# Performance work log

Hardware: AMD Instinct MI355X
Metric: run time of the kernel (lower is better)

Reference implementation:

```python
import jax, jax.numpy as jnp
import numpy as np
from jax import lax

NVOX = 100
EPS = 1e-4
DN = ('NDHWC', 'DHWIO', 'NDHWC')

# scn semantics emulated densely: inactive voxels are identically zero and the
# active-site mask is re-applied after every layer, so submanifold convolution,
# strided sparse conv, sparse deconv and masked BN-ReLU compute the same values
# at active sites as SparseConvNet's rulebook gather-GEMM-scatter.

def _bnrelu(x, p, mask):
    # p: [4, C] = (gamma, beta, running_mean, running_var); inference-form BN.
    g, b, mu, v = p[0], p[1], p[2], p[3]
    return jax.nn.relu((x - mu) * (g * lax.rsqrt(v + EPS)) + b) * mask

def _subconv(x, w, mask):
    # Submanifold conv: inputs outside active set are zero; outputs only at active sites.
    return lax.conv_general_dilated(x, w, (1, 1, 1), 'SAME', dimension_numbers=DN) * mask

def _down(x, w):
    # scn.Convolution(dim, a, b, size=2, stride=2, bias=False)
    return lax.conv_general_dilated(x, w, (2, 2, 2), 'VALID', dimension_numbers=DN)

def _up(x, w, mask):
    # scn.Deconvolution restores the pre-downsample active set -> mask with finer mask.
    return lax.conv_transpose(x, w, (2, 2, 2), 'VALID', dimension_numbers=DN) * mask

def _pool_mask(mask):
    return lax.reduce_window(mask, 0.0, lax.max, (1, 2, 2, 2, 1), (1, 2, 2, 2, 1), 'VALID')

def _forward(coords, feats, w_in, w0a, wdown0, w1a, wdown1, w2, wup1, w1post, wup0, w0post,
             bnA, bnB, bnC, bnD, bnE, bnF, bnG, bnH, bnI, bnJ, linW, linb):
    i, j, k = coords[:, 0], coords[:, 1], coords[:, 2]
    # InputLayer mode=3: sum features at duplicate coordinates.
    grid = jnp.zeros((1, NVOX, NVOX, NVOX, 1), feats.dtype).at[0, i, j, k, 0].add(feats[:, 0])
    mask0 = jnp.zeros((1, NVOX, NVOX, NVOX, 1), feats.dtype).at[0, i, j, k, 0].set(1.0)
    mask1 = _pool_mask(mask0)   # 50^3 active set after strided conv
    mask2 = _pool_mask(mask1)   # 25^3

    x = _subconv(grid, w_in, mask0)                          # 1 -> 32
    x0 = _subconv(_bnrelu(x, bnA, mask0), w0a, mask0)        # level-0 VGG block
    d0 = _down(_bnrelu(x0, bnB, mask0), wdown0)              # 32 -> 64, 100 -> 50
    x1 = _subconv(_bnrelu(d0, bnC, mask1), w1a, mask1)       # level-1 VGG block
    d1 = _down(_bnrelu(x1, bnD, mask1), wdown1)              # 64 -> 96, 50 -> 25
    x2 = _subconv(_bnrelu(d1, bnE, mask2), w2, mask2)        # level-2 VGG block
    u1 = _up(_bnrelu(x2, bnF, mask2), wup1, mask1)           # 96 -> 64, 25 -> 50
    y1 = _subconv(_bnrelu(jnp.concatenate([x1, u1], -1), bnG, mask1), w1post, mask1)  # 128 -> 64
    u0 = _up(_bnrelu(y1, bnH, mask1), wup0, mask0)           # 64 -> 32, 50 -> 100
    y0 = _subconv(_bnrelu(jnp.concatenate([x0, u0], -1), bnI, mask0), w0post, mask0)  # 64 -> 32
    y = _bnrelu(y0, bnJ, mask0)                              # final BatchNormReLU(32)
    pts = y[0, i, j, k, :]                                   # OutputLayer: gather active sites [N,32]
    return pts @ linW + linb                                 # Linear(32, 3)


def setup_inputs() -> dict:
    key = jax.random.key(0)
    ks = jax.random.split(key, 24)
    N = 120000
    coords = jax.random.randint(ks[0], (N, 3), 0, NVOX, dtype=jnp.int32)
    feats = jax.random.normal(ks[1], (N, 1), jnp.float32)

    def w(k, shape, fan_in):
        return (jax.random.normal(k, shape, jnp.float32) / np.float32(np.sqrt(fan_in)))

    def bn(k, c):
        k1, k2, k3, k4 = jax.random.split(k, 4)
        return jnp.stack([
            1.0 + 0.1 * jax.random.normal(k1, (c,)),
            0.1 * jax.random.normal(k2, (c,)),
            0.1 * jax.random.normal(k3, (c,)),
            0.5 + jax.random.uniform(k4, (c,)),
        ]).astype(jnp.float32)

    return dict(
        coords=coords, feats=feats,
        w_in=w(ks[2], (3, 3, 3, 1, 32), 27),
        w0a=w(ks[3], (3, 3, 3, 32, 32), 27 * 32),
        wdown0=w(ks[4], (2, 2, 2, 32, 64), 8 * 32),
        w1a=w(ks[5], (3, 3, 3, 64, 64), 27 * 64),
        wdown1=w(ks[6], (2, 2, 2, 64, 96), 8 * 64),
        w2=w(ks[7], (3, 3, 3, 96, 96), 27 * 96),
        wup1=w(ks[8], (2, 2, 2, 96, 64), 96),
        w1post=w(ks[9], (3, 3, 3, 128, 64), 27 * 128),
        wup0=w(ks[10], (2, 2, 2, 64, 32), 64),
        w0post=w(ks[11], (3, 3, 3, 64, 32), 27 * 64),
        bnA=bn(ks[12], 32), bnB=bn(ks[13], 32), bnC=bn(ks[14], 64), bnD=bn(ks[15], 64),
        bnE=bn(ks[16], 96), bnF=bn(ks[17], 96), bnG=bn(ks[18], 128), bnH=bn(ks[19], 64),
        bnI=bn(ks[20], 64), bnJ=bn(ks[21], 32),
        linW=w(ks[22], (32, 3), 32),
        linb=0.01 * jax.random.normal(ks[23], (3,), jnp.float32),
    )


def reference(coords, feats, w_in, w0a, wdown0, w1a, wdown1, w2, wup1, w1post, wup0, w0post,
              bnA, bnB, bnC, bnD, bnE, bnF, bnG, bnH, bnI, bnJ, linW, linb):
    return _forward(coords, feats, w_in, w0a, wdown0, w1a, wdown1, w2, wup1, w1post, wup0, w0post,
                    bnA, bnB, bnC, bnD, bnE, bnF, bnG, bnH, bnI, bnJ, linW, linb)
```

## Files before the change

kernel.cpp:

```cpp
#include <hip/hip_runtime.h>


#define NVOX 100
#define EPSB 1e-4f
typedef unsigned long long u64;
typedef _Float16 h2 __attribute__((ext_vector_type(2)));
typedef _Float16 h8 __attribute__((ext_vector_type(8)));
typedef float f16v __attribute__((ext_vector_type(16)));
#define DEVFN __device__ __forceinline__

DEVFN float bnr(float v, float sc, float sh) { return fmaxf(fmaf(v, sc, sh), 0.f); }

template<int NTAPS, int CTOT, int COUT>
__global__ __launch_bounds__(256)
void prepB32(const float* __restrict__ w, h2* __restrict__ out)
{
    constexpr int CTG = COUT / 32, KCH = CTOT / 16;
    const int n = NTAPS * CTG * KCH * 256;
    const int idx = blockIdx.x * 256 + threadIdx.x;
    if (idx >= n) return;
    const int jh = idx & 3;
    const int lane = (idx >> 2) & 63;
    int r = idx >> 8;
    const int kc = r % KCH; r /= KCH;
    const int ct = r % CTG; const int t = r / CTG;
    const int k0 = kc * 16 + (lane >> 5) * 8 + 2 * jh;
    const int co = ct * 32 + (lane & 31);
    h2 v;
    v[0] = (_Float16)w[((size_t)t * CTOT + k0) * COUT + co];
    v[1] = (_Float16)w[((size_t)t * CTOT + k0 + 1) * COUT + co];
    out[idx] = v;
}

template<int EMODE, int COUT>
DEVFN void epilogue(float a, int srow, int ch,
                    float* outF, _Float16* o1, const float* sc1, const float* sh1,
                    _Float16* o2, const float* sc2, const float* sh2)
{
    if constexpr (EMODE == 0) {
        outF[(size_t)srow * COUT + ch] = a;
    } else {
        o1[(size_t)srow * COUT + ch] = (_Float16)bnr(a, sc1[ch], sh1[ch]);
        if constexpr (EMODE == 2)
            o2[(size_t)srow * COUT + ch] = (_Float16)bnr(a, sc2[ch], sh2[ch]);
    }
}

template<int KC1, int KC2, int CTILES, int COUT, int S, int EMODE>
__global__ __launch_bounds__(64)
void gconv_m32(const h2* __restrict__ inA, const h2* __restrict__ inB,
               const h2* __restrict__ wb,
               const int* __restrict__ amap, const int* __restrict__ vlist,
               const int* __restrict__ cnt, int cap, int nbx,
               float* __restrict__ outF, _Float16* __restrict__ o1,
               const float* __restrict__ sc1, const float* __restrict__ sh1,
               _Float16* __restrict__ o2,
               const float* __restrict__ sc2, const float* __restrict__ sh2)
{
    constexpr int KCH = KC1 + KC2;
    constexpr int CTG = COUT / 32;
    const int lane = threadIdx.x;
    const int cntv = *cnt;
    const int sid = blockIdx.x;
    const int ct0 = sid / nbx;
    const int wbase = (sid - ct0 * nbx) * 32;
    if (wbase >= cntv) return;
    const int l31 = lane & 31, ksub = lane >> 5;
    const int slot = wbase + l31;
    const bool on = slot < cntv;
    int X = 0, Y = 0, Z = 0;
    if (on) { const int v = vlist[slot]; X = v % S; const int r = v / S; Y = r % S; Z = r / S; }

    auto calc_ns = [&](int t) -> int {
        int ns = cap;
        if (on) {
            const int dz = t / 9 - 1, dy = (t / 3) % 3 - 1, dx = t % 3 - 1;
            const int nz = Z + dz, ny = Y + dy, nx = X + dx;
            if ((unsigned)nz < (unsigned)S && (unsigned)ny < (unsigned)S &&
                (unsigned)nx < (unsigned)S) {
                const int m = amap[(nz * S + ny) * S + nx];
                if (m >= 0) ns = m;
            }
        }
        return ns;
    };

    f16v acc[CTILES];
#pragma unroll
    for (int c = 0; c < CTILES; ++c) acc[c] = (f16v)(0.f);
    int ns = calc_ns(0);
#pragma unroll 1
    for (int t = 0; t < 27; ++t) {
        const int ns_nxt = (t + 1 < 27) ? calc_ns(t + 1) : cap;
        const h2* __restrict__ wt =
            wb + ((size_t)t * CTG + ct0 * CTILES) * KCH * 256;
#pragma unroll
        for (int kc = 0; kc < KC1; ++kc) {
            const h8 a = *reinterpret_cast<const h8*>(
                inA + (size_t)ns * (KC1 * 8) + kc * 8 + ksub * 4);
#pragma unroll
            for (int ct = 0; ct < CTILES; ++ct) {
                const h8 b = *reinterpret_cast<const h8*>(
                    wt + ((size_t)ct * KCH + kc) * 256 + lane * 4);
                acc[ct] = __builtin_amdgcn_mfma_f32_32x32x16_f16(a, b, acc[ct], 0, 0, 0);
            }
        }
        if constexpr (KC2 > 0) {
#pragma unroll
            for (int kc = 0; kc < KC2; ++kc) {
                const h8 a = *reinterpret_cast<const h8*>(
                    inB + (size_t)ns * (KC2 * 8) + kc * 8 + ksub * 4);
#pragma unroll
                for (int ct = 0; ct < CTILES; ++ct) {
                    const h8 b = *reinterpret_cast<const h8*>(
                        wt + ((size_t)ct * KCH + KC1 + kc) * 256 + lane * 4);
                    acc[ct] = __builtin_amdgcn_mfma_f32_32x32x16_f16(a, b, acc[ct], 0, 0, 0);
                }
            }
        }
        ns = ns_nxt;
    }
#pragma unroll
    for (int ct = 0; ct < CTILES; ++ct) {
        const int ch = (ct0 * CTILES + ct) * 32 + l31;
#pragma unroll
        for (int r = 0; r < 16; ++r) {
            const int row = (r & 3) + 8 * (r >> 2) + 4 * ksub;
            const int srow = wbase + row;
            if (srow < cntv)
                epilogue<EMODE, COUT>(acc[ct][r], srow, ch, outF, o1, sc1, sh1,
                                      o2, sc2, sh2);
        }
    }
}

template<int KCH, int CTILES, int COUT, int SC>
__global__ __launch_bounds__(64)
void dconv_m32(const h2* __restrict__ in, const h2* __restrict__ wb,
               const int* __restrict__ amap_f, const int* __restrict__ vlist_c,
               const int* __restrict__ cnt_c, int capf, int nbx,
               _Float16* __restrict__ o1,
               const float* __restrict__ sc1, const float* __restrict__ sh1)
{
    constexpr int SF = SC * 2;
    constexpr int CTG = COUT / 32;
    const int lane = threadIdx.x;
    const int cntv = *cnt_c;
    const int sid = blockIdx.x;
    const int ct0 = sid / nbx;
    const int wbase = (sid - ct0 * nbx) * 32;
    if (wbase >= cntv) return;
    const int l31 = lane & 31, ksub = lane >> 5;
    const int slot = wbase + l31;
    const bool on = slot < cntv;
    int X = 0, Y = 0, Z = 0;
    if (on) { const int v = vlist_c[slot]; X = v % SC; const int r = v / SC; Y = r % SC; Z = r / SC; }

    auto calc_ns = [&](int t) -> int {
        int ns = capf;
        if (on) {
            const int fz = 2 * Z + ((t >> 2) & 1);
            const int fy = 2 * Y + ((t >> 1) & 1);
            const int fx = 2 * X + (t & 1);
            const int m = amap_f[(fz * SF + fy) * SF + fx];
            if (m >= 0) ns = m;
        }
        return ns;
    };

    f16v acc[CTILES];
#pragma unroll
    for (int c = 0; c < CTILES; ++c) acc[c] = (f16v)(0.f);
    int ns = calc_ns(0);
#pragma unroll 1
    for (int t = 0; t < 8; ++t) {
        const int ns_nxt = (t + 1 < 8) ? calc_ns(t + 1) : capf;
        const h2* __restrict__ wt =
            wb + ((size_t)t * CTG + ct0 * CTILES) * KCH * 256;
#pragma unroll
        for (int kc = 0; kc < KCH; ++kc) {
            const h8 a = *reinterpret_cast<const h8*>(
                in + (size_t)ns * (KCH * 8) + kc * 8 + ksub * 4);
#pragma unroll
            for (int ct = 0; ct < CTILES; ++ct) {
                const h8 b = *reinterpret_cast<const h8*>(
                    wt + ((size_t)ct * KCH + kc) * 256 + lane * 4);
                acc[ct] = __builtin_amdgcn_mfma_f32_32x32x16_f16(a, b, acc[ct], 0, 0, 0);
            }
        }
        ns = ns_nxt;
    }
#pragma unroll
    for (int ct = 0; ct < CTILES; ++ct) {
        const int ch = (ct0 * CTILES + ct) * 32 + l31;
#pragma unroll
        for (int r = 0; r < 16; ++r) {
            const int row = (r & 3) + 8 * (r >> 2) + 4 * ksub;
            const int srow = wbase + row;
            if (srow < cntv)
                o1[(size_t)srow * COUT + ch] =
                    (_Float16)bnr(acc[ct][r], sc1[ch], sh1[ch]);
        }
    }
}

template<int KCH, int CTILES, int COUT, int SC>
__global__ __launch_bounds__(64)
void uconv_m32(const h2* __restrict__ in, const h2* __restrict__ wb,
               const int* __restrict__ amap_f, const int* __restrict__ vlist_c,
               const int* __restrict__ cnt_c, int cap, int nbx,
               _Float16* __restrict__ out,
               const float* __restrict__ sc, const float* __restrict__ sh)
{
    constexpr int SF = SC * 2;
    constexpr int CTG = COUT / 32;
    const int lane = threadIdx.x;
    const int cntv = *cnt_c;
    const int sid = blockIdx.x;
    const int ct0 = sid / nbx;
    const int wbase = (sid - ct0 * nbx) * 32;
    if (wbase >= cntv) return;
    const int l31 = lane & 31, ksub = lane >> 5;
    const int slot = wbase + l31;
    const bool on = slot < cntv;
    int X = 0, Y = 0, Z = 0;
    if (on) { const int v = vlist_c[slot]; X = v % SC; const int r = v / SC; Y = r % SC; Z = r / SC; }

    h8 a[KCH];
    const int arow = on ? slot : cap;
#pragma unroll
    for (int kc = 0; kc < KCH; ++kc)
        a[kc] = *reinterpret_cast<const h8*>(
            in + (size_t)arow * (KCH * 8) + kc * 8 + ksub * 4);

    auto calc_cs = [&](int t) -> int {
        int cs = -1;
        if (on) {
            const int fz = 2 * Z + ((t >> 2) & 1);
            const int fy = 2 * Y + ((t >> 1) & 1);
            const int fx = 2 * X + (t & 1);
            cs = amap_f[(fz * SF + fy) * SF + fx];
        }
        return cs;
    };

    int cs = calc_cs(0);
#pragma unroll 1
    for (int t = 0; t < 8; ++t) {
        const int cs_nxt = (t + 1 < 8) ? calc_cs(t + 1) : -1;
        const h2* __restrict__ wt =
            wb + ((size_t)(7 - t) * CTG + ct0 * CTILES) * KCH * 256;
        f16v acc[CTILES];
#pragma unroll
        for (int c = 0; c < CTILES; ++c) acc[c] = (f16v)(0.f);
#pragma unroll
        for (int kc = 0; kc < KCH; ++kc) {
#pragma unroll
            for (int ct = 0; ct < CTILES; ++ct) {
                const h8 b = *reinterpret_cast<const h8*>(
                    wt + ((size_t)ct * KCH + kc) * 256 + lane * 4);
                acc[ct] = __builtin_amdgcn_mfma_f32_32x32x16_f16(a[kc], b, acc[ct], 0, 0, 0);
            }
        }
#pragma unroll
        for (int ct = 0; ct < CTILES; ++ct) {
            const int ch = (ct0 * CTILES + ct) * 32 + l31;
#pragma unroll
            for (int r = 0; r < 16; ++r) {
                const int row = (r & 3) + 8 * (r >> 2) + 4 * ksub;
                const int csr = __shfl(cs, row, 64);
                if (csr >= 0)
                    out[(size_t)csr * COUT + ch] =
                        (_Float16)bnr(acc[ct][r], sc[ch], sh[ch]);
            }
        }
        cs = cs_nxt;
    }
}

template<int S>
__global__ __launch_bounds__(128)
void cin_k(const float* __restrict__ grid, const float* __restrict__ w,
           const int* __restrict__ vlist, const int* __restrict__ cnt,
           _Float16* __restrict__ out, const float* __restrict__ sc,
           const float* __restrict__ sh)
{
    const int wOff = __builtin_amdgcn_readfirstlane(threadIdx.x >> 6) * 16;
    const int slot = blockIdx.x * 64 + (threadIdx.x & 63);
    if (slot >= *cnt) return;
    const int v = vlist[slot];
    const int x = v % S;
    const int rem = v / S;
    const int y = rem % S;
    const int z = rem / S;
    float acc[16];
#pragma unroll
    for (int c = 0; c < 16; ++c) acc[c] = 0.f;
#pragma unroll
    for (int t = 0; t < 27; ++t) {
        const int dz = t / 9 - 1, dy = (t / 3) % 3 - 1, dx = t % 3 - 1;
        const int nz = z + dz, ny = y + dy, nx = x + dx;
        if ((unsigned)nz >= (unsigned)S || (unsigned)ny >= (unsigned)S ||
            (unsigned)nx >= (unsigned)S) continue;
        const float val = grid[(nz * S + ny) * S + nx];
        const float* __restrict__ wp = w + t * 32 + wOff;
#pragma unroll
        for (int c = 0; c < 16; ++c) acc[c] = fmaf(val, wp[c], acc[c]);
    }
    union { float4 v[2]; _Float16 h[16]; } o;
#pragma unroll
    for (int c = 0; c < 16; ++c)
        o.h[c] = (_Float16)bnr(acc[c], sc[wOff + c], sh[wOff + c]);
    float4* dst = reinterpret_cast<float4*>(out + (size_t)slot * 32 + wOff);
    dst[0] = o.v[0];
    dst[1] = o.v[1];
}

__global__ __launch_bounds__(256)
void final_k(const int* __restrict__ coords, const float* __restrict__ y0,
             const int* __restrict__ amap0, const float* __restrict__ ssJ,
             const float* __restrict__ linW, const float* __restrict__ linb,
             int N, float* __restrict__ outp)
{
    const int n = blockIdx.x * blockDim.x + threadIdx.x;
    if (n >= N) return;
    const int i = coords[3 * n + 0];
    const int j = coords[3 * n + 1];
    const int k = coords[3 * n + 2];
    const int v = (i * NVOX + j) * NVOX + k;
    const int s = amap0[v];
    float a0 = linb[0], a1 = linb[1], a2 = linb[2];
    if (s >= 0) {
        const float* __restrict__ row = y0 + (size_t)s * 32;
#pragma unroll
        for (int c = 0; c < 32; ++c) {
            const float t = bnr(row[c], ssJ[c], ssJ[32 + c]);
            a0 = fmaf(t, linW[c * 3 + 0], a0);
            a1 = fmaf(t, linW[c * 3 + 1], a1);
            a2 = fmaf(t, linW[c * 3 + 2], a2);
        }
    }
    outp[3 * n + 0] = a0;
    outp[3 * n + 1] = a1;
    outp[3 * n + 2] = a2;
}

__global__ void bn_prep(const float* __restrict__ A, const float* __restrict__ B,
                        const float* __restrict__ C, const float* __restrict__ D,
                        const float* __restrict__ E, const float* __restrict__ F,
                        const float* __restrict__ G, const float* __restrict__ H,
                        const float* __restrict__ I, const float* __restrict__ J,
                        float* __restrict__ ss)
{
    const float* bp[10] = {A, B, C, D, E, F, G, H, I, J};
    const int CH[10] = {32, 32, 64, 64, 96, 96, 128, 64, 64, 32};
    int idx = blockIdx.x * blockDim.x + threadIdx.x;
    if (idx >= 672) return;
    int l = 0, base = 0, off2 = 0;
    while (idx >= base + CH[l]) { base += CH[l]; off2 += 2 * CH[l]; ++l; }
    const int c = idx - base;
    const float* bn = bp[l];
    const int Cc = CH[l];
    const float g = bn[c], b = bn[Cc + c], mu = bn[2 * Cc + c], var = bn[3 * Cc + c];
    const float sc = g * rsqrtf(var + EPSB);
    ss[off2 + c] = sc;
    ss[off2 + Cc + c] = b - mu * sc;
}

__global__ __launch_bounds__(256)
void scatter_mark(const int* __restrict__ coords, const float* __restrict__ feats,
                  int N, float* __restrict__ grid, int* __restrict__ amap0)
{
    const int n = blockIdx.x * blockDim.x + threadIdx.x;
    if (n >= N) return;
    const int i = coords[3 * n + 0];
    const int j = coords[3 * n + 1];
    const int k = coords[3 * n + 2];
    const int v = (i * NVOX + j) * NVOX + k;
    atomicAdd(&grid[v], feats[n]);
    amap0[v] = -2;
}

template<int SC>
__global__ __launch_bounds__(256)
void flag_coarse(const int* __restrict__ amap_f, int* __restrict__ amap_c)
{
    constexpr int SF = SC * 2;
    const int v = blockIdx.x * blockDim.x + threadIdx.x;
    if (v >= SC * SC * SC) return;
    const int x = v % SC;
    const int rem = v / SC;
    const int y = rem % SC;
    const int z = rem / SC;
    bool any = false;
#pragma unroll
    for (int t = 0; t < 8; ++t) {
        const int fz = 2 * z + ((t >> 2) & 1);
        const int fy = 2 * y + ((t >> 1) & 1);
        const int fx = 2 * x + (t & 1);
        if (amap_f[(fz * SF + fy) * SF + fx] >= 0) any = true;
    }
    amap_c[v] = any ? -2 : -1;
}

__global__ __launch_bounds__(256)
void count_k(const int* __restrict__ flags, int V, int* __restrict__ counts)
{
    const int v = blockIdx.x * 256 + threadIdx.x;
    const bool act = (v < V) && (flags[v] == -2);
    const u64 m = __ballot(act);
    __shared__ int c[4];
    const int wid = threadIdx.x >> 6;
    if ((threadIdx.x & 63) == 0) c[wid] = __popcll(m);
    __syncthreads();
    if (threadIdx.x == 0) counts[blockIdx.x] = c[0] + c[1] + c[2] + c[3];
}

__global__ __launch_bounds__(1024)
void scan_k(int* __restrict__ counts, int nb, int* __restrict__ total)
{
    __shared__ int sums[1024];
    const int t = threadIdx.x;
    int v[4];
    int s = 0;
#pragma unroll
    for (int i = 0; i < 4; ++i) {
        const int idx = t * 4 + i;
        v[i] = (idx < nb) ? counts[idx] : 0;
        s += v[i];
    }
    sums[t] = s;
    __syncthreads();
    for (int d = 1; d < 1024; d <<= 1) {
        const int add = (t >= d) ? sums[t - d] : 0;
        __syncthreads();
        sums[t] += add;
        __syncthreads();
    }
    int base = (t > 0) ? sums[t - 1] : 0;
#pragma unroll
    for (int i = 0; i < 4; ++i) {
        const int idx = t * 4 + i;
        if (idx < nb) counts[idx] = base;
        base += v[i];
    }
    if (t == 1023) *total = sums[1023];
}

__global__ __launch_bounds__(256)
void emit_k(int* __restrict__ amap, int V, const int* __restrict__ offsets,
            int* __restrict__ vlist)
{
    const int v = blockIdx.x * 256 + threadIdx.x;
    const bool act = (v < V) && (amap[v] == -2);
    const u64 m = __ballot(act);
    __shared__ int wbase[4];
    const int wid = threadIdx.x >> 6;
    const int lane = threadIdx.x & 63;
    if (lane == 0) wbase[wid] = __popcll(m);
    __syncthreads();
    if (threadIdx.x == 0) {
        int s = 0;
#pragma unroll
        for (int i = 0; i < 4; ++i) { const int t = wbase[i]; wbase[i] = s; s += t; }
    }
    __syncthreads();
    if (act) {
        const int slot = offsets[blockIdx.x] + wbase[wid] +
                         __popcll(m & ((1ull << lane) - 1ull));
        amap[v] = slot;
        vlist[slot] = v;
    }
}

extern "C" void kernel_launch(void* const* d_in, const int* in_sizes, int n_in,
                              void* d_out, int out_size, void* d_ws, size_t ws_size,
                              hipStream_t stream) {
    const int*   coords = (const int*)d_in[0];
    const float* feats  = (const float*)d_in[1];
    const float* w_in   = (const float*)d_in[2];
    const float* w0a    = (const float*)d_in[3];
    const float* wdown0 = (const float*)d_in[4];
    const float* w1a    = (const float*)d_in[5];
    const float* wdown1 = (const float*)d_in[6];
    const float* w2     = (const float*)d_in[7];
    const float* wup1   = (const float*)d_in[8];
    const float* w1post = (const float*)d_in[9];
    const float* wup0   = (const float*)d_in[10];
    const float* w0post = (const float*)d_in[11];
    const float* linW = (const float*)d_in[22];
    const float* linb = (const float*)d_in[23];
    float* outp = (float*)d_out;

    const int N = in_sizes[1];
    const int V0 = NVOX * NVOX * NVOX;
    const int V1 = 50 * 50 * 50;
    const int V2 = 25 * 25 * 25;
    const int cap0 = N;
    const int cap1 = 100000;
    const int cap2 = V2;

    char* ws = (char*)d_ws;
    size_t off = 0;
    auto alloc = [&](size_t bytes) -> void* {
        void* p = ws + off;
        off += (bytes + 255) & ~(size_t)255;
        return p;
    };
    int*   amap0  = (int*)alloc((size_t)V0 * 4);
    int*   vlist0 = (int*)alloc((size_t)cap0 * 4);
    int*   amap1  = (int*)alloc((size_t)V1 * 4);
    int*   vlist1 = (int*)alloc((size_t)cap1 * 4);
    int*   amap2  = (int*)alloc((size_t)V2 * 4);
    int*   vlist2 = (int*)alloc((size_t)cap2 * 4);
    int*   cnt    = (int*)alloc(3 * 4);
    int*   counts = (int*)alloc(4096 * 4);
    float* ss     = (float*)alloc(1344 * 4);
    float* grid   = (float*)alloc((size_t)V0 * 4);
    _Float16* HA  = (_Float16*)alloc((size_t)(cap0 + 1) * 32 * 2);
    _Float16* HB  = (_Float16*)alloc((size_t)(cap0 + 1) * 32 * 2);
    _Float16* HI1 = (_Float16*)alloc((size_t)(cap0 + 1) * 32 * 2);
    _Float16* HI2 = (_Float16*)alloc((size_t)(cap0 + 1) * 32 * 2);
    _Float16* HC  = (_Float16*)alloc((size_t)(cap1 + 1) * 64 * 2);
    _Float16* HD  = (_Float16*)alloc((size_t)(cap1 + 1) * 64 * 2);
    _Float16* HG1 = (_Float16*)alloc((size_t)(cap1 + 1) * 64 * 2);
    _Float16* HG2 = (_Float16*)alloc((size_t)(cap1 + 1) * 64 * 2);
    _Float16* HE  = (_Float16*)alloc((size_t)(cap2 + 1) * 96 * 2);
    _Float16* HF  = (_Float16*)alloc((size_t)(cap2 + 1) * 96 * 2);
    _Float16* HH  = (_Float16*)alloc((size_t)(cap1 + 1) * 64 * 2);
    float* y0f  = (float*)alloc((size_t)cap0 * 32 * 4);
    h2* wbA  = (h2*)alloc((size_t)27 * 1 * 2 * 256 * 4);
    h2* wb1  = (h2*)alloc((size_t)27 * 2 * 4 * 256 * 4);
    h2* wb2  = (h2*)alloc((size_t)27 * 3 * 6 * 256 * 4);
    h2* wbP1 = (h2*)alloc((size_t)27 * 2 * 8 * 256 * 4);
    h2* wbP0 = (h2*)alloc((size_t)27 * 1 * 4 * 256 * 4);
    h2* wbD0 = (h2*)alloc((size_t)8 * 2 * 2 * 256 * 4);
    h2* wbD1 = (h2*)alloc((size_t)8 * 3 * 4 * 256 * 4);
    h2* wbU1 = (h2*)alloc((size_t)8 * 2 * 6 * 256 * 4);
    h2* wbU0 = (h2*)alloc((size_t)8 * 1 * 4 * 256 * 4);
    if (off > ws_size) return;

    const int B = 256;
    const int gN  = (N + B - 1) / B;
    const int nb0 = (V0 + B - 1) / B;
    const int nb1 = (V1 + B - 1) / B;
    const int nb2 = (V2 + B - 1) / B;
    const int sb0 = (cap0 + 63) / 64;
    const int g1w_0 = (cap0 + 31) / 32;
    const int g1w_1 = (cap1 + 31) / 32;
    const int g1w_2 = (cap2 + 31) / 32;

    hipMemsetAsync(amap0, 0xFF, (size_t)V0 * 4, stream);
    hipMemsetAsync(grid, 0, (size_t)V0 * 4, stream);
    hipMemsetAsync(HA + (size_t)cap0 * 32, 0, 64, stream);
    hipMemsetAsync(HB + (size_t)cap0 * 32, 0, 64, stream);
    hipMemsetAsync(HI1 + (size_t)cap0 * 32, 0, 64, stream);
    hipMemsetAsync(HI2 + (size_t)cap0 * 32, 0, 64, stream);
    hipMemsetAsync(HC + (size_t)cap1 * 64, 0, 128, stream);
    hipMemsetAsync(HD + (size_t)cap1 * 64, 0, 128, stream);
    hipMemsetAsync(HG1 + (size_t)cap1 * 64, 0, 128, stream);
    hipMemsetAsync(HG2 + (size_t)cap1 * 64, 0, 128, stream);
    hipMemsetAsync(HE + (size_t)cap2 * 96, 0, 192, stream);
    hipMemsetAsync(HF + (size_t)cap2 * 96, 0, 192, stream);
    hipMemsetAsync(HH + (size_t)cap1 * 64, 0, 128, stream);
    bn_prep<<<3, 256, 0, stream>>>((const float*)d_in[12], (const float*)d_in[13],
                                   (const float*)d_in[14], (const float*)d_in[15],
                                   (const float*)d_in[16], (const float*)d_in[17],
                                   (const float*)d_in[18], (const float*)d_in[19],
                                   (const float*)d_in[20], (const float*)d_in[21], ss);
    prepB32<27, 32, 32><<<(27 * 1 * 2 * 256 + 255) / 256, 256, 0, stream>>>(w0a, wbA);
    prepB32<27, 64, 64><<<(27 * 2 * 4 * 256 + 255) / 256, 256, 0, stream>>>(w1a, wb1);
    prepB32<27, 96, 96><<<(27 * 3 * 6 * 256 + 255) / 256, 256, 0, stream>>>(w2, wb2);
    prepB32<27, 128, 64><<<(27 * 2 * 8 * 256 + 255) / 256, 256, 0, stream>>>(w1post, wbP1);
    prepB32<27, 64, 32><<<(27 * 1 * 4 * 256 + 255) / 256, 256, 0, stream>>>(w0post, wbP0);
    prepB32<8, 32, 64><<<(8 * 2 * 2 * 256 + 255) / 256, 256, 0, stream>>>(wdown0, wbD0);
    prepB32<8, 64, 96><<<(8 * 3 * 4 * 256 + 255) / 256, 256, 0, stream>>>(wdown1, wbD1);
    prepB32<8, 96, 64><<<(8 * 2 * 6 * 256 + 255) / 256, 256, 0, stream>>>(wup1, wbU1);
    prepB32<8, 64, 32><<<(8 * 1 * 4 * 256 + 255) / 256, 256, 0, stream>>>(wup0, wbU0);
    scatter_mark<<<gN, B, 0, stream>>>(coords, feats, N, grid, amap0);
    count_k<<<nb0, B, 0, stream>>>(amap0, V0, counts);
    scan_k<<<1, 1024, 0, stream>>>(counts, nb0, cnt + 0);
    emit_k<<<nb0, B, 0, stream>>>(amap0, V0, counts, vlist0);
    flag_coarse<50><<<nb1, B, 0, stream>>>(amap0, amap1);
    count_k<<<nb1, B, 0, stream>>>(amap1, V1, counts);
    scan_k<<<1, 1024, 0, stream>>>(counts, nb1, cnt + 1);
    emit_k<<<nb1, B, 0, stream>>>(amap1, V1, counts, vlist1);
    flag_coarse<25><<<nb2, B, 0, stream>>>(amap1, amap2);
    count_k<<<nb2, B, 0, stream>>>(amap2, V2, counts);
    scan_k<<<1, 1024, 0, stream>>>(counts, nb2, cnt + 2);
    emit_k<<<nb2, B, 0, stream>>>(amap2, V2, counts, vlist2);

    cin_k<100><<<sb0, 128, 0, stream>>>(grid, w_in, vlist0, cnt + 0, HA,
                                        ss + 0, ss + 32);
    gconv_m32<2, 0, 1, 32, 100, 2><<<g1w_0, 64, 0, stream>>>(
        (const h2*)HA, nullptr, wbA, amap0, vlist0, cnt + 0, cap0, g1w_0,
        nullptr, HB, ss + 64, ss + 96, HI1, ss + 1152, ss + 1216);
    dconv_m32<2, 2, 64, 50><<<g1w_1, 64, 0, stream>>>(
        (const h2*)HB, wbD0, amap0, vlist1, cnt + 1, cap0, g1w_1,
        HC, ss + 128, ss + 192);
    gconv_m32<4, 0, 2, 64, 50, 2><<<g1w_1, 64, 0, stream>>>(
        (const h2*)HC, nullptr, wb1, amap1, vlist1, cnt + 1, cap1, g1w_1,
        nullptr, HD, ss + 256, ss + 320, HG1, ss + 768, ss + 896);
    dconv_m32<4, 1, 96, 25><<<g1w_2 * 3, 64, 0, stream>>>(
        (const h2*)HD, wbD1, amap1, vlist2, cnt + 2, cap1, g1w_2,
        HE, ss + 384, ss + 480);
    gconv_m32<6, 0, 1, 96, 25, 1><<<g1w_2 * 3, 64, 0, stream>>>(
        (const h2*)HE, nullptr, wb2, amap2, vlist2, cnt + 2, cap2, g1w_2,
        nullptr, HF, ss + 576, ss + 672, nullptr, nullptr, nullptr);
    uconv_m32<6, 2, 64, 25><<<g1w_2, 64, 0, stream>>>(
        (const h2*)HF, wbU1, amap1, vlist2, cnt + 2, cap2, g1w_2,
        HG2, ss + 768 + 64, ss + 896 + 64);
    gconv_m32<4, 4, 2, 64, 50, 1><<<g1w_1, 64, 0, stream>>>(
        (const h2*)HG1, (const h2*)HG2, wbP1, amap1, vlist1, cnt + 1, cap1, g1w_1,
        nullptr, HH, ss + 1024, ss + 1088, nullptr, nullptr, nullptr);
    uconv_m32<4, 1, 32, 50><<<g1w_1, 64, 0, stream>>>(
        (const h2*)HH, wbU0, amap0, vlist1, cnt + 1, cap1, g1w_1,
        HI2, ss + 1152 + 32, ss + 1216 + 32);
    gconv_m32<2, 2, 1, 32, 100, 0><<<g1w_0, 64, 0, stream>>>(
        (const h2*)HI1, (const h2*)HI2, wbP0, amap0, vlist0, cnt + 0, cap0, g1w_0,
        y0f, nullptr, nullptr, nullptr, nullptr, nullptr, nullptr);
    final_k<<<gN, B, 0, stream>>>(coords, y0f, amap0, ss + 1280, linW, linb, N, outp);
}
```

Measured before the change: 447.7 us.

## Use dense voxel indexing at coarse levels instead of compacted active lists

Levels 1 and 2 (50^3 and 25^3) now store features densely, indexed by voxel, instead of through compacted vlist/count/scan arrays. Convolutions run over every coarse voxel and zero inactive outputs with a wave ballot on the active mask. This removes the count/scan/emit passes and the amap indirection on neighbour lookups. The cost is that all 125k and 15.6k voxels are computed even when the active set is sparse, which adds MFMA work and memory traffic.

```diff
diff --git a/kernel.cpp b/kernel.cpp
--- a/kernel.cpp
+++ b/kernel.cpp
@@ -32,21 +32,7 @@
     out[idx] = v;
 }
 
-template<int EMODE, int COUT>
-DEVFN void epilogue(float a, int srow, int ch,
-                    float* outF, _Float16* o1, const float* sc1, const float* sh1,
-                    _Float16* o2, const float* sc2, const float* sh2)
-{
-    if constexpr (EMODE == 0) {
-        outF[(size_t)srow * COUT + ch] = a;
-    } else {
-        o1[(size_t)srow * COUT + ch] = (_Float16)bnr(a, sc1[ch], sh1[ch]);
-        if constexpr (EMODE == 2)
-            o2[(size_t)srow * COUT + ch] = (_Float16)bnr(a, sc2[ch], sh2[ch]);
-    }
-}
-
-template<int KC1, int KC2, int CTILES, int COUT, int S, int EMODE>
+template<int KC1, int KC2, int CTILES, int COUT, int S, int EMODE, bool DENSE>
 __global__ __launch_bounds__(64)
 void gconv_m32(const h2* __restrict__ inA, const h2* __restrict__ inB,
                const h2* __restrict__ wb,
@@ -60,7 +46,7 @@
     constexpr int KCH = KC1 + KC2;
     constexpr int CTG = COUT / 32;
     const int lane = threadIdx.x;
-    const int cntv = *cnt;
+    const int cntv = DENSE ? S * S * S : *cnt;
     const int sid = blockIdx.x;
     const int ct0 = sid / nbx;
     const int wbase = (sid - ct0 * nbx) * 32;
@@ -69,7 +55,12 @@
     const int slot = wbase + l31;
     const bool on = slot < cntv;
     int X = 0, Y = 0, Z = 0;
-    if (on) { const int v = vlist[slot]; X = v % S; const int r = v / S; Y = r % S; Z = r / S; }
+    if (on) {
+        const int v = DENSE ? slot : vlist[slot];
+        X = v % S; const int r = v / S; Y = r % S; Z = r / S;
+    }
+    u64 bal = 0;
+    if constexpr (DENSE) bal = __ballot(on && amap[slot] >= 0);
 
     auto calc_ns = [&](int t) -> int {
         int ns = cap;
@@ -78,8 +69,12 @@
             const int nz = Z + dz, ny = Y + dy, nx = X + dx;
             if ((unsigned)nz < (unsigned)S && (unsigned)ny < (unsigned)S &&
                 (unsigned)nx < (unsigned)S) {
-                const int m = amap[(nz * S + ny) * S + nx];
-                if (m >= 0) ns = m;
+                if constexpr (DENSE) {
+                    ns = (nz * S + ny) * S + nx;
+                } else {
+                    const int m = amap[(nz * S + ny) * S + nx];
+                    if (m >= 0) ns = m;
+                }
             }
         }
         return ns;
@@ -127,34 +122,50 @@
         for (int r = 0; r < 16; ++r) {
             const int row = (r & 3) + 8 * (r >> 2) + 4 * ksub;
             const int srow = wbase + row;
-            if (srow < cntv)
-                epilogue<EMODE, COUT>(acc[ct][r], srow, ch, outF, o1, sc1, sh1,
-                                      o2, sc2, sh2);
-        }
-    }
-}
-
-template<int KCH, int CTILES, int COUT, int SC>
+            if (srow < cntv) {
+                if constexpr (EMODE == 0) {
+                    outF[(size_t)srow * COUT + ch] = acc[ct][r];
+                } else if constexpr (DENSE) {
+                    const bool mk = (bal >> row) & 1;
+                    o1[(size_t)srow * COUT + ch] =
+                        mk ? (_Float16)bnr(acc[ct][r], sc1[ch], sh1[ch]) : (_Float16)0.f;
+                    if constexpr (EMODE == 2)
+                        o2[(size_t)srow * COUT + ch] =
+                            mk ? (_Float16)bnr(acc[ct][r], sc2[ch], sh2[ch]) : (_Float16)0.f;
+                } else {
+                    o1[(size_t)srow * COUT + ch] =
+                        (_Float16)bnr(acc[ct][r], sc1[ch], sh1[ch]);
+                    if constexpr (EMODE == 2)
+                        o2[(size_t)srow * COUT + ch] =
+                            (_Float16)bnr(acc[ct][r], sc2[ch], sh2[ch]);
+                }
+            }
+        }
+    }
+}
+
+template<int KCH, int CTILES, int COUT, int SC, bool CHILD_SPARSE>
 __global__ __launch_bounds__(64)
 void dconv_m32(const h2* __restrict__ in, const h2* __restrict__ wb,
-               const int* __restrict__ amap_f, const int* __restrict__ vlist_c,
-               const int* __restrict__ cnt_c, int capf, int nbx,
+               const int* __restrict__ amap_f, const int* __restrict__ amap_cm,
+               int capf, int nbx,
                _Float16* __restrict__ o1,
                const float* __restrict__ sc1, const float* __restrict__ sh1)
 {
     constexpr int SF = SC * 2;
     constexpr int CTG = COUT / 32;
+    constexpr int VC = SC * SC * SC;
     const int lane = threadIdx.x;
-    const int cntv = *cnt_c;
     const int sid = blockIdx.x;
     const int ct0 = sid / nbx;
     const int wbase = (sid - ct0 * nbx) * 32;
-    if (wbase >= cntv) return;
+    if (wbase >= VC) return;
     const int l31 = lane & 31, ksub = lane >> 5;
     const int slot = wbase + l31;
-    const bool on = slot < cntv;
+    const bool on = slot < VC;
     int X = 0, Y = 0, Z = 0;
-    if (on) { const int v = vlist_c[slot]; X = v % SC; const int r = v / SC; Y = r % SC; Z = r / SC; }
+    if (on) { X = slot % SC; const int r = slot / SC; Y = r % SC; Z = r / SC; }
+    const u64 bal = __ballot(on && amap_cm[on ? slot : 0] >= 0);
 
     auto calc_ns = [&](int t) -> int {
         int ns = capf;
@@ -162,8 +173,13 @@
             const int fz = 2 * Z + ((t >> 2) & 1);
             const int fy = 2 * Y + ((t >> 1) & 1);
             const int fx = 2 * X + (t & 1);
-            const int m = amap_f[(fz * SF + fy) * SF + fx];
-            if (m >= 0) ns = m;
+            const int fi = (fz * SF + fy) * SF + fx;
+            if constexpr (CHILD_SPARSE) {
+                const int m = amap_f[fi];
+                if (m >= 0) ns = m;
+            } else {
+                ns = fi;
+            }
         }
         return ns;
     };
@@ -197,57 +213,71 @@
         for (int r = 0; r < 16; ++r) {
             const int row = (r & 3) + 8 * (r >> 2) + 4 * ksub;
             const int srow = wbase + row;
-            if (srow < cntv)
+            if (srow < VC) {
+                const bool mk = (bal >> row) & 1;
                 o1[(size_t)srow * COUT + ch] =
-                    (_Float16)bnr(acc[ct][r], sc1[ch], sh1[ch]);
-        }
-    }
-}
-
-template<int KCH, int CTILES, int COUT, int SC>
+                    mk ? (_Float16)bnr(acc[ct][r], sc1[ch], sh1[ch]) : (_Float16)0.f;
+            }
+        }
+    }
+}
+
+template<int KCH, int CTILES, int COUT, int SC, bool CHILD_SPARSE>
 __global__ __launch_bounds__(64)
 void uconv_m32(const h2* __restrict__ in, const h2* __restrict__ wb,
-               const int* __restrict__ amap_f, const int* __restrict__ vlist_c,
-               const int* __restrict__ cnt_c, int cap, int nbx,
+               const int* __restrict__ amap_f, const int* __restrict__ amap_cm,
+               int capIn, int nbx,
                _Float16* __restrict__ out,
                const float* __restrict__ sc, const float* __restrict__ sh)
 {
     constexpr int SF = SC * 2;
     constexpr int CTG = COUT / 32;
+    constexpr int VC = SC * SC * SC;
     const int lane = threadIdx.x;
-    const int cntv = *cnt_c;
     const int sid = blockIdx.x;
     const int ct0 = sid / nbx;
     const int wbase = (sid - ct0 * nbx) * 32;
-    if (wbase >= cntv) return;
+    if (wbase >= VC) return;
     const int l31 = lane & 31, ksub = lane >> 5;
     const int slot = wbase + l31;
-    const bool on = slot < cntv;
+    const bool on = slot < VC;
     int X = 0, Y = 0, Z = 0;
-    if (on) { const int v = vlist_c[slot]; X = v % SC; const int r = v / SC; Y = r % SC; Z = r / SC; }
+    if (on) { X = slot % SC; const int r = slot / SC; Y = r % SC; Z = r / SC; }
 
     h8 a[KCH];
-    const int arow = on ? slot : cap;
+    const int arow = on ? slot : capIn;
 #pragma unroll
     for (int kc = 0; kc < KCH; ++kc)
         a[kc] = *reinterpret_cast<const h8*>(
             in + (size_t)arow * (KCH * 8) + kc * 8 + ksub * 4);
 
-    auto calc_cs = [&](int t) -> int {
+    auto calc_cs = [&](int t, bool& mk) -> int {
         int cs = -1;
+        mk = false;
         if (on) {
             const int fz = 2 * Z + ((t >> 2) & 1);
             const int fy = 2 * Y + ((t >> 1) & 1);
             const int fx = 2 * X + (t & 1);
-            cs = amap_f[(fz * SF + fy) * SF + fx];
+            const int fi = (fz * SF + fy) * SF + fx;
+            if constexpr (CHILD_SPARSE) {
+                cs = amap_f[fi];
+                mk = cs >= 0;
+            } else {
+                cs = fi;
+                mk = amap_cm[fi] >= 0;
+            }
         }
         return cs;
     };
 
-    int cs = calc_cs(0);
+    bool mk;
+    int cs = calc_cs(0, mk);
 #pragma unroll 1
     for (int t = 0; t < 8; ++t) {
-        const int cs_nxt = (t + 1 < 8) ? calc_cs(t + 1) : -1;
+        bool mk_nxt = false;
+        const int cs_nxt = (t + 1 < 8) ? calc_cs(t + 1, mk_nxt) : -1;
+        const u64 balw = __ballot(on && (CHILD_SPARSE ? (cs >= 0) : true));
+        const u64 balm = __ballot(mk);
         const h2* __restrict__ wt =
             wb + ((size_t)(7 - t) * CTG + ct0 * CTILES) * KCH * 256;
         f16v acc[CTILES];
@@ -269,12 +299,15 @@
             for (int r = 0; r < 16; ++r) {
                 const int row = (r & 3) + 8 * (r >> 2) + 4 * ksub;
                 const int csr = __shfl(cs, row, 64);
-                if (csr >= 0)
+                const bool wok = (balw >> row) & 1;
+                const bool mrk = (balm >> row) & 1;
+                if (wok)
                     out[(size_t)csr * COUT + ch] =
-                        (_Float16)bnr(acc[ct][r], sc[ch], sh[ch]);
+                        mrk ? (_Float16)bnr(acc[ct][r], sc[ch], sh[ch]) : (_Float16)0.f;
             }
         }
         cs = cs_nxt;
+        mk = mk_nxt;
     }
 }
 
@@ -400,7 +433,7 @@
         const int fx = 2 * x + (t & 1);
         if (amap_f[(fz * SF + fy) * SF + fx] >= 0) any = true;
     }
-    amap_c[v] = any ? -2 : -1;
+    amap_c[v] = any ? 1 : -1;
 }
 
 __global__ __launch_bounds__(256)
@@ -497,8 +530,6 @@
     const int V1 = 50 * 50 * 50;
     const int V2 = 25 * 25 * 25;
     const int cap0 = N;
-    const int cap1 = 100000;
-    const int cap2 = V2;
 
     char* ws = (char*)d_ws;
     size_t off = 0;
@@ -510,9 +541,7 @@
     int*   amap0  = (int*)alloc((size_t)V0 * 4);
     int*   vlist0 = (int*)alloc((size_t)cap0 * 4);
     int*   amap1  = (int*)alloc((size_t)V1 * 4);
-    int*   vlist1 = (int*)alloc((size_t)cap1 * 4);
     int*   amap2  = (int*)alloc((size_t)V2 * 4);
-    int*   vlist2 = (int*)alloc((size_t)cap2 * 4);
     int*   cnt    = (int*)alloc(3 * 4);
     int*   counts = (int*)alloc(4096 * 4);
     float* ss     = (float*)alloc(1344 * 4);
@@ -521,13 +550,13 @@
     _Float16* HB  = (_Float16*)alloc((size_t)(cap0 + 1) * 32 * 2);
     _Float16* HI1 = (_Float16*)alloc((size_t)(cap0 + 1) * 32 * 2);
     _Float16* HI2 = (_Float16*)alloc((size_t)(cap0 + 1) * 32 * 2);
-    _Float16* HC  = (_Float16*)alloc((size_t)(cap1 + 1) * 64 * 2);
-    _Float16* HD  = (_Float16*)alloc((size_t)(cap1 + 1) * 64 * 2);
-    _Float16* HG1 = (_Float16*)alloc((size_t)(cap1 + 1) * 64 * 2);
-    _Float16* HG2 = (_Float16*)alloc((size_t)(cap1 + 1) * 64 * 2);
-    _Float16* HE  = (_Float16*)alloc((size_t)(cap2 + 1) * 96 * 2);
-    _Float16* HF  = (_Float16*)alloc((size_t)(cap2 + 1) * 96 * 2);
-    _Float16* HH  = (_Float16*)alloc((size_t)(cap1 + 1) * 64 * 2);
+    _Float16* HC  = (_Float16*)alloc((size_t)(V1 + 1) * 64 * 2);
+    _Float16* HD  = (_Float16*)alloc((size_t)(V1 + 1) * 64 * 2);
+    _Float16* HG1 = (_Float16*)alloc((size_t)(V1 + 1) * 64 * 2);
+    _Float16* HG2 = (_Float16*)alloc((size_t)(V1 + 1) * 64 * 2);
+    _Float16* HH  = (_Float16*)alloc((size_t)(V1 + 1) * 64 * 2);
+    _Float16* HE  = (_Float16*)alloc((size_t)(V2 + 1) * 96 * 2);
+    _Float16* HF  = (_Float16*)alloc((size_t)(V2 + 1) * 96 * 2);
     float* y0f  = (float*)alloc((size_t)cap0 * 32 * 4);
     h2* wbA  = (h2*)alloc((size_t)27 * 1 * 2 * 256 * 4);
     h2* wb1  = (h2*)alloc((size_t)27 * 2 * 4 * 256 * 4);
@@ -547,8 +576,8 @@
     const int nb2 = (V2 + B - 1) / B;
     const int sb0 = (cap0 + 63) / 64;
     const int g1w_0 = (cap0 + 31) / 32;
-    const int g1w_1 = (cap1 + 31) / 32;
-    const int g1w_2 = (cap2 + 31) / 32;
+    const int gd1   = (V1 + 31) / 32;
+    const int gd2   = (V2 + 31) / 32;
 
     hipMemsetAsync(amap0, 0xFF, (size_t)V0 * 4, stream);
     hipMemsetAsync(grid, 0, (size_t)V0 * 4, stream);
@@ -556,13 +585,13 @@
     hipMemsetAsync(HB + (size_t)cap0 * 32, 0, 64, stream);
     hipMemsetAsync(HI1 + (size_t)cap0 * 32, 0, 64, stream);
     hipMemsetAsync(HI2 + (size_t)cap0 * 32, 0, 64, stream);
-    hipMemsetAsync(HC + (size_t)cap1 * 64, 0, 128, stream);
-    hipMemsetAsync(HD + (size_t)cap1 * 64, 0, 128, stream);
-    hipMemsetAsync(HG1 + (size_t)cap1 * 64, 0, 128, stream);
-    hipMemsetAsync(HG2 + (size_t)cap1 * 64, 0, 128, stream);
-    hipMemsetAsync(HE + (size_t)cap2 * 96, 0, 192, stream);
-    hipMemsetAsync(HF + (size_t)cap2 * 96, 0, 192, stream);
-    hipMemsetAsync(HH + (size_t)cap1 * 64, 0, 128, stream);
+    hipMemsetAsync(HC + (size_t)V1 * 64, 0, 128, stream);
+    hipMemsetAsync(HD + (size_t)V1 * 64, 0, 128, stream);
+    hipMemsetAsync(HG1 + (size_t)V1 * 64, 0, 128, stream);
+    hipMemsetAsync(HG2 + (size_t)V1 * 64, 0, 128, stream);
+    hipMemsetAsync(HH + (size_t)V1 * 64, 0, 128, stream);
+    hipMemsetAsync(HE + (size_t)V2 * 96, 0, 192, stream);
+    hipMemsetAsync(HF + (size_t)V2 * 96, 0, 192, stream);
     bn_prep<<<3, 256, 0, stream>>>((const float*)d_in[12], (const float*)d_in[13],
                                    (const float*)d_in[14], (const float*)d_in[15],
                                    (const float*)d_in[16], (const float*)d_in[17],
@@ -582,41 +611,33 @@
     scan_k<<<1, 1024, 0, stream>>>(counts, nb0, cnt + 0);
     emit_k<<<nb0, B, 0, stream>>>(amap0, V0, counts, vlist0);
     flag_coarse<50><<<nb1, B, 0, stream>>>(amap0, amap1);
-    count_k<<<nb1, B, 0, stream>>>(amap1, V1, counts);
-    scan_k<<<1, 1024, 0, stream>>>(counts, nb1, cnt + 1);
-    emit_k<<<nb1, B, 0, stream>>>(amap1, V1, counts, vlist1);
     flag_coarse<25><<<nb2, B, 0, stream>>>(amap1, amap2);
-    count_k<<<nb2, B, 0, stream>>>(amap2, V2, counts);
-    scan_k<<<1, 1024, 0, stream>>>(counts, nb2, cnt + 2);
-    emit_k<<<nb2, B, 0, stream>>>(amap2, V2, counts, vlist2);
 
     cin_k<100><<<sb0, 128, 0, stream>>>(grid, w_in, vlist0, cnt + 0, HA,
                                         ss + 0, ss + 32);
-    gconv_m32<2, 0, 1, 32, 100, 2><<<g1w_0, 64, 0, stream>>>(
+    gconv_m32<2, 0, 1, 32, 100, 2, false><<<g1w_0, 64, 0, stream>>>(
         (const h2*)HA, nullptr, wbA, amap0, vlist0, cnt + 0, cap0, g1w_0,
         nullptr, HB, ss + 64, ss + 96, HI1, ss + 1152, ss + 1216);
-    dconv_m32<2, 2, 64, 50><<<g1w_1, 64, 0, stream>>>(
-        (const h2*)HB, wbD0, amap0, vlist1, cnt + 1, cap0, g1w_1,
-        HC, ss + 128, ss + 192);
-    gconv_m32<4, 0, 2, 64, 50, 2><<<g1w_1, 64, 0, stream>>>(
-        (const h2*)HC, nullptr, wb1, amap1, vlist1, cnt + 1, cap1, g1w_1,
+    dconv_m32<2, 2, 64, 50, true><<<gd1, 64, 0, stream>>>(
+        (const h2*)HB, wbD0, amap0, amap1, cap0, gd1, HC, ss + 128, ss + 192);
+    gconv_m32<4, 0, 2, 64, 50, 2, true><<<gd1, 64, 0, stream>>>(
+        (const h2*)HC, nullptr, wb1, amap1, nullptr, nullptr, V1, gd1,
         nullptr, HD, ss + 256, ss + 320, HG1, ss + 768, ss + 896);
-    dconv_m32<4, 1, 96, 25><<<g1w_2 * 3, 64, 0, stream>>>(
-        (const h2*)HD, wbD1, amap1, vlist2, cnt + 2, cap1, g1w_2,
-        HE, ss + 384, ss + 480);
-    gconv_m32<6, 0, 1, 96, 25, 1><<<g1w_2 * 3, 64, 0, stream>>>(
-        (const h2*)HE, nullptr, wb2, amap2, vlist2, cnt + 2, cap2, g1w_2,
+    dconv_m32<4, 1, 96, 25, false><<<gd2 * 3, 64, 0, stream>>>(
+        (const h2*)HD, wbD1, nullptr, amap2, V1, gd2, HE, ss + 384, ss + 480);
+    gconv_m32<6, 0, 1, 96, 25, 1, true><<<gd2 * 3, 64, 0, stream>>>(
+        (const h2*)HE, nullptr, wb2, amap2, nullptr, nullptr, V2, gd2,
         nullptr, HF, ss + 576, ss + 672, nullptr, nullptr, nullptr);
-    uconv_m32<6, 2, 64, 25><<<g1w_2, 64, 0, stream>>>(
-        (const h2*)HF, wbU1, amap1, vlist2, cnt + 2, cap2, g1w_2,
+    uconv_m32<6, 2, 64, 25, false><<<gd2, 64, 0, stream>>>(
+        (const h2*)HF, wbU1, nullptr, amap1, V2, gd2,
         HG2, ss + 768 + 64, ss + 896 + 64);
-    gconv_m32<4, 4, 2, 64, 50, 1><<<g1w_1, 64, 0, stream>>>(
-        (const h2*)HG1, (const h2*)HG2, wbP1, amap1, vlist1, cnt + 1, cap1, g1w_1,
+    gconv_m32<4, 4, 2, 64, 50, 1, true><<<gd1, 64, 0, stream>>>(
+        (const h2*)HG1, (const h2*)HG2, wbP1, amap1, nullptr, nullptr, V1, gd1,
         nullptr, HH, ss + 1024, ss + 1088, nullptr, nullptr, nullptr);
-    uconv_m32<4, 1, 32, 50><<<g1w_1, 64, 0, stream>>>(
-        (const h2*)HH, wbU0, amap0, vlist1, cnt + 1, cap1, g1w_1,
+    uconv_m32<4, 1, 32, 50, true><<<gd1, 64, 0, stream>>>(
+        (const h2*)HH, wbU0, amap0, nullptr, V1, gd1,
         HI2, ss + 1152 + 32, ss + 1216 + 32);
-    gconv_m32<2, 2, 1, 32, 100, 0><<<g1w_0, 64, 0, stream>>>(
+    gconv_m32<2, 2, 1, 32, 100, 0, false><<<g1w_0, 64, 0, stream>>>(
         (const h2*)HI1, (const h2*)HI2, wbP0, amap0, vlist0, cnt + 0, cap0, g1w_0,
         y0f, nullptr, nullptr, nullptr, nullptr, nullptr, nullptr);
     final_k<<<gN, B, 0, stream>>>(coords, y0f, amap0, ss + 1280, linW, linb, N, outp);
```

Result: slower. 553.6 us (+23.6%).
